# Optimization experiments

Measured on AMD Instinct MI355X. Metric: run time of the kernel, lower is better.

## Reference

```python
import jax, jax.numpy as jnp
import numpy as np

N_NODES = 46080   # 512 graphs x 90 nodes
NPG = 90          # nodes per graph (AAL atlas)
G = 512           # number of graphs
E = 737280        # edges (degree 16)
IN_DIM = 90
H = 64            # hidden_channels
K = 70            # sort-pool k


def setup_inputs() -> dict:
    key = jax.random.key(0)
    ks = jax.random.split(key, 12)
    x = jax.random.normal(ks[0], (N_NODES, IN_DIM), dtype=jnp.float32)
    # intra-graph random edges: src/dst within each graph's 90-node block
    gidx = jnp.repeat(jnp.arange(G, dtype=jnp.int64), E // G) * NPG
    src = jax.random.randint(ks[1], (E,), 0, NPG, dtype=jnp.int64) + gidx
    dst = jax.random.randint(ks[2], (E,), 0, NPG, dtype=jnp.int64) + gidx
    edge_index = jnp.stack([src, dst])
    edge_weight = jax.random.uniform(ks[3], (E,), dtype=jnp.float32)
    batch = jnp.repeat(jnp.arange(G, dtype=jnp.int64), NPG)
    s1 = 1.0 / np.sqrt(IN_DIM)
    s2 = 1.0 / np.sqrt(H)
    sk = 1.0 / np.sqrt(H * K)
    W1 = jax.random.uniform(ks[4], (IN_DIM, H), jnp.float32, -s1, s1)
    b1 = jnp.zeros((H,), jnp.float32)
    W2 = jax.random.uniform(ks[5], (H, H), jnp.float32, -s2, s2)
    b2 = jnp.zeros((H,), jnp.float32)
    lw1 = jax.random.uniform(ks[6], (H * K, H), jnp.float32, -sk, sk)
    lb1 = jax.random.uniform(ks[7], (H,), jnp.float32, -sk, sk)
    lw2 = jax.random.uniform(ks[8], (H, 1), jnp.float32, -s2, s2)
    lb2 = jax.random.uniform(ks[9], (1,), jnp.float32, -s2, s2)
    return {"x": x, "edge_index": edge_index, "edge_weight": edge_weight,
            "batch": batch, "W1": W1, "b1": b1, "W2": W2, "b2": b2,
            "lw1": lw1, "lb1": lb1, "lw2": lw2, "lb2": lb2}


def _gcn_conv(x, W, b, src, dst, ew, n):
    # PyG GCNConv: add self-loops (weight 1), symmetric normalization,
    # message = norm * (x @ W)[src], scatter-add to dst, add bias.
    xw = x @ W
    loop = jnp.arange(n)
    src_f = jnp.concatenate([src, loop])
    dst_f = jnp.concatenate([dst, loop])
    ew_f = jnp.concatenate([ew, jnp.ones((n,), x.dtype)])
    deg = jax.ops.segment_sum(ew_f, dst_f, num_segments=n)
    dinv = jnp.where(deg > 0, jax.lax.rsqrt(jnp.maximum(deg, 1e-12)), 0.0)
    norm = dinv[src_f] * ew_f * dinv[dst_f]
    msg = xw[src_f] * norm[:, None]          # [E+n, H] irregular gather
    out = jax.ops.segment_sum(msg, dst_f, num_segments=n)
    return out + b


def reference(x, edge_index, edge_weight, batch, W1, b1, W2, b2, lw1, lb1, lw2, lb2):
    src, dst = edge_index[0], edge_index[1]
    h1 = _gcn_conv(x, W1, b1, src, dst, edge_weight, N_NODES)
    x_train = h1
    h = jax.nn.relu(h1)
    h2 = _gcn_conv(h, W2, b2, src, dst, edge_weight, N_NODES)
    # global_sort_pool: per graph, sort nodes descending by last channel, keep top K.
    # batch is contiguous with NPG nodes/graph, so a reshape is exact.
    hg = h2.reshape(G, NPG, H)
    order = jnp.argsort(-hg[:, :, -1], axis=1)          # [G, NPG] descending
    hs = jnp.take_along_axis(hg, order[:, :, None], axis=1)
    pooled = hs[:, :K, :].reshape(G, K * H)
    # F.dropout(p=0.5, training=False) -> identity at inference
    z = pooled @ lw1 + lb1
    z = z @ lw2 + lb2
    out = jax.nn.sigmoid(z).squeeze(-1)                  # [G]
    return out, x_train
```

## Files before the change

kernel.cpp:

```cpp
#include <hip/hip_runtime.h>


#define NG      512
#define NPG     90
#define EPG     1440
#define IN_DIM  90
#define HD      64
#define KP      70
#define E_TOT   (NG*EPG)
#define NT      512

__global__ __launch_bounds__(NT, 4) void dgcnn_fused(
    const float* __restrict__ x,
    const int*   __restrict__ ei,
    const float* __restrict__ ew,
    const float* __restrict__ W1,
    const float* __restrict__ b1,
    const float* __restrict__ W2,
    const float* __restrict__ b2,
    const float* __restrict__ lw1,
    const float* __restrict__ lb1,
    const float* __restrict__ lw2,
    const float* __restrict__ lb2,
    float* __restrict__ out,
    float* __restrict__ xtrain)
{
    __shared__ float sB[NPG*HD];
    __shared__ float sC[NPG*HD];
    __shared__ float sW2[HD*HD];
    __shared__ float s_deg[NPG];
    __shared__ float s_dinv[NPG];
    __shared__ int   s_indeg[NPG];
    __shared__ int   s_rowstart[NPG+1];
    __shared__ int   s_cursor[NPG];
    __shared__ float2 s_cpack[EPG];
    __shared__ int   s_ranknode[KP];
    __shared__ float s_zpart[NT];

    const int g = blockIdx.x;
    const int t = threadIdx.x;
    const int j = t & 63;
    const int grp = t >> 6;
    const int ebase = g*EPG;
    const int nbase = g*NPG;

    if (t < NPG) { s_deg[t] = 1.0f; s_indeg[t] = 0; }
    __syncthreads();

    for (int e = t; e < EPG; e += NT) {
        int d = ei[E_TOT + ebase + e] - nbase;
        float w = ew[ebase + e];
        atomicAdd(&s_deg[d], w);
        atomicAdd(&s_indeg[d], 1);
    }
    __syncthreads();

    if (t < NPG) s_dinv[t] = rsqrtf(fmaxf(s_deg[t], 1e-12f));
    if (t <= NPG) {
        int acc = 0;
        for (int i = 0; i < t; ++i) acc += s_indeg[i];
        s_rowstart[t] = acc;
        if (t < NPG) s_cursor[t] = acc;
    }
    __syncthreads();

    for (int e = t; e < EPG; e += NT) {
        int s = ei[ebase + e] - nbase;
        int d = ei[E_TOT + ebase + e] - nbase;
        float w = ew[ebase + e];
        int pos = atomicAdd(&s_cursor[d], 1);
        s_cpack[pos] = make_float2(s_dinv[s] * w * s_dinv[d], __int_as_float(s));
    }
    for (int i4 = t; i4 < IN_DIM*HD/4; i4 += NT)
        ((float4*)sC)[i4] = ((const float4*)W1)[i4];
    __syncthreads();

    const float* xg = x + (size_t)nbase * IN_DIM;
    for (int it = 0; it < 3; ++it) {
        int r0 = it*32 + grp*4;
        int rr0 = min(r0+0, NPG-1), rr1 = min(r0+1, NPG-1);
        int rr2 = min(r0+2, NPG-1), rr3 = min(r0+3, NPG-1);
        const float2* xp0 = (const float2*)(xg + rr0*IN_DIM);
        const float2* xp1 = (const float2*)(xg + rr1*IN_DIM);
        const float2* xp2 = (const float2*)(xg + rr2*IN_DIM);
        const float2* xp3 = (const float2*)(xg + rr3*IN_DIM);
        float a0 = 0.f, a1 = 0.f, a2 = 0.f, a3 = 0.f;
        #pragma unroll 9
        for (int kh = 0; kh < IN_DIM/2; ++kh) {
            float w0 = sC[(2*kh)*HD + j];
            float w1 = sC[(2*kh+1)*HD + j];
            float2 v0 = xp0[kh], v1 = xp1[kh], v2 = xp2[kh], v3 = xp3[kh];
            a0 += v0.x*w0 + v0.y*w1;
            a1 += v1.x*w0 + v1.y*w1;
            a2 += v2.x*w0 + v2.y*w1;
            a3 += v3.x*w0 + v3.y*w1;
        }
        if (r0+0 < NPG) sB[(r0+0)*HD + j] = a0;
        if (r0+1 < NPG) sB[(r0+1)*HD + j] = a1;
        if (r0+2 < NPG) sB[(r0+2)*HD + j] = a2;
        if (r0+3 < NPG) sB[(r0+3)*HD + j] = a3;
    }
    __syncthreads();

    for (int o = t; o < NPG*HD; o += NT) {
        int d = o >> 6, c = o & 63;
        float dv = s_dinv[d];
        float a = dv*dv*sB[o];
        int p0 = s_rowstart[d], p1 = s_rowstart[d+1];
        for (int p = p0; p < p1; ++p) {
            float2 pk = s_cpack[p];
            a += pk.x * sB[__float_as_int(pk.y)*HD + c];
        }
        sC[o] = a + b1[c];
    }
    __syncthreads();

    float* xt = xtrain + (size_t)nbase * HD;
    for (int i4 = t; i4 < NPG*HD/4; i4 += NT) {
        float4 v = ((float4*)sC)[i4];
        ((float4*)xt)[i4] = v;
        v.x = fmaxf(v.x, 0.f); v.y = fmaxf(v.y, 0.f);
        v.z = fmaxf(v.z, 0.f); v.w = fmaxf(v.w, 0.f);
        ((float4*)sC)[i4] = v;
    }
    for (int i4 = t; i4 < HD*HD/4; i4 += NT)
        ((float4*)sW2)[i4] = ((const float4*)W2)[i4];
    __syncthreads();

    for (int it = 0; it < 3; ++it) {
        int r0 = it*32 + grp*4;
        int rr0 = min(r0+0, NPG-1), rr1 = min(r0+1, NPG-1);
        int rr2 = min(r0+2, NPG-1), rr3 = min(r0+3, NPG-1);
        float a0 = 0.f, a1 = 0.f, a2 = 0.f, a3 = 0.f;
        #pragma unroll 4
        for (int k4 = 0; k4 < HD/4; ++k4) {
            int k = k4*4;
            float4 h0 = *(const float4*)&sC[rr0*HD + k];
            float4 h1 = *(const float4*)&sC[rr1*HD + k];
            float4 h2 = *(const float4*)&sC[rr2*HD + k];
            float4 h3 = *(const float4*)&sC[rr3*HD + k];
            float w0 = sW2[(k+0)*HD + j];
            float w1 = sW2[(k+1)*HD + j];
            float w2 = sW2[(k+2)*HD + j];
            float w3 = sW2[(k+3)*HD + j];
            a0 += h0.x*w0 + h0.y*w1 + h0.z*w2 + h0.w*w3;
            a1 += h1.x*w0 + h1.y*w1 + h1.z*w2 + h1.w*w3;
            a2 += h2.x*w0 + h2.y*w1 + h2.z*w2 + h2.w*w3;
            a3 += h3.x*w0 + h3.y*w1 + h3.z*w2 + h3.w*w3;
        }
        if (r0+0 < NPG) sB[(r0+0)*HD + j] = a0;
        if (r0+1 < NPG) sB[(r0+1)*HD + j] = a1;
        if (r0+2 < NPG) sB[(r0+2)*HD + j] = a2;
        if (r0+3 < NPG) sB[(r0+3)*HD + j] = a3;
    }
    __syncthreads();

    for (int o = t; o < NPG*HD; o += NT) {
        int d = o >> 6, c = o & 63;
        float dv = s_dinv[d];
        float a = dv*dv*sB[o];
        int p0 = s_rowstart[d], p1 = s_rowstart[d+1];
        for (int p = p0; p < p1; ++p) {
            float2 pk = s_cpack[p];
            a += pk.x * sB[__float_as_int(pk.y)*HD + c];
        }
        sC[o] = a + b2[c];
    }
    __syncthreads();

    if (t < NPG) {
        float vi = sC[t*HD + (HD-1)];
        int rank = 0;
        for (int jj = 0; jj < NPG; ++jj) {
            float vj = sC[jj*HD + (HD-1)];
            rank += (vj > vi) || (vj == vi && jj < t);
        }
        if (rank < KP) s_ranknode[rank] = t;
    }
    __syncthreads();

    {
        float partial = 0.f;
        for (int k = grp; k < KP; k += 8) {
            int node = s_ranknode[k];
            const float4* prow = (const float4*)&sC[node*HD];
            const float* wrow = lw1 + (size_t)(k*HD)*HD + j;
            #pragma unroll 4
            for (int c4 = 0; c4 < HD/4; ++c4) {
                float4 pv = prow[c4];
                int c = c4*4;
                partial += pv.x * wrow[(size_t)(c+0)*HD];
                partial += pv.y * wrow[(size_t)(c+1)*HD];
                partial += pv.z * wrow[(size_t)(c+2)*HD];
                partial += pv.w * wrow[(size_t)(c+3)*HD];
            }
        }
        s_zpart[t] = partial;
    }
    __syncthreads();

    if (t < HD) {
        float z1 = lb1[t];
        #pragma unroll
        for (int m = 0; m < NT/HD; ++m) z1 += s_zpart[t + m*HD];
        float zz = z1 * lw2[t];
        #pragma unroll
        for (int off = 32; off > 0; off >>= 1) zz += __shfl_down(zz, off, 64);
        if (t == 0) out[g] = 1.0f / (1.0f + expf(-(zz + lb2[0])));
    }
}

extern "C" void kernel_launch(void* const* d_in, const int* in_sizes, int n_in,
                              void* d_out, int out_size, void* d_ws, size_t ws_size,
                              hipStream_t stream) {
    const float* x   = (const float*)d_in[0];
    const int*   ei  = (const int*)  d_in[1];
    const float* ew  = (const float*)d_in[2];
    const float* W1  = (const float*)d_in[4];
    const float* b1  = (const float*)d_in[5];
    const float* W2  = (const float*)d_in[6];
    const float* b2  = (const float*)d_in[7];
    const float* lw1 = (const float*)d_in[8];
    const float* lb1 = (const float*)d_in[9];
    const float* lw2 = (const float*)d_in[10];
    const float* lb2 = (const float*)d_in[11];

    float* out    = (float*)d_out;
    float* xtrain = out + NG;

    dgcnn_fused<<<NG, NT, 0, stream>>>(x, ei, ew, W1, b1, W2, b2,
                                       lw1, lb1, lw2, lb2, out, xtrain);
}
```

Baseline: 192.7 us.

## Fold the two dense head layers into one vector and slim the shared-memory footprint

A small pre-kernel folds lw1·lw2 and the biases into one effective weight vector, since no nonlinearity sits between the two head layers. The per-graph head then becomes a single dot product instead of a 4480x64 matrix-vector product streamed from global memory. Shared memory is also reduced to allow more blocks per CU: edge norm and source index are packed into one 32-bit word by truncating the low 7 mantissa bits of the norm, the W2 shared copy is dropped in favour of global/L1 reads, and the xtrain store is fused into the aggregation loop. Edge data is kept in registers between passes. The costs are an extra launch, a small loss of precision in the norm, and a changed summation order.

```diff
diff --git a/kernel.cpp b/kernel.cpp
--- a/kernel.cpp
+++ b/kernel.cpp
@@ -10,7 +10,30 @@
 #define E_TOT   (NG*EPG)
 #define NT      512
 
-__global__ __launch_bounds__(NT, 4) void dgcnn_fused(
+__global__ __launch_bounds__(256) void weff_fold(
+    const float* __restrict__ lw1, const float* __restrict__ lb1,
+    const float* __restrict__ lw2, const float* __restrict__ lb2,
+    float* __restrict__ ws)
+{
+    int i = blockIdx.x*256 + threadIdx.x;
+    if (i < KP*HD) {
+        const float4* row = (const float4*)(lw1 + (size_t)i*HD);
+        const float4* w   = (const float4*)lw2;
+        float s = 0.f;
+        #pragma unroll
+        for (int j4 = 0; j4 < HD/4; ++j4) {
+            float4 r = row[j4], v = w[j4];
+            s += r.x*v.x + r.y*v.y + r.z*v.z + r.w*v.w;
+        }
+        ws[i] = s;
+    } else if (i == KP*HD) {
+        float s = lb2[0];
+        for (int j = 0; j < HD; ++j) s += lb1[j]*lw2[j];
+        ws[KP*HD] = s;
+    }
+}
+
+__global__ __launch_bounds__(NT, 6) void dgcnn_fused(
     const float* __restrict__ x,
     const int*   __restrict__ ei,
     const float* __restrict__ ew,
@@ -18,24 +41,18 @@
     const float* __restrict__ b1,
     const float* __restrict__ W2,
     const float* __restrict__ b2,
-    const float* __restrict__ lw1,
-    const float* __restrict__ lb1,
-    const float* __restrict__ lw2,
-    const float* __restrict__ lb2,
+    const float* __restrict__ weff,
     float* __restrict__ out,
     float* __restrict__ xtrain)
 {
     __shared__ float sB[NPG*HD];
     __shared__ float sC[NPG*HD];
-    __shared__ float sW2[HD*HD];
-    __shared__ float s_deg[NPG];
     __shared__ float s_dinv[NPG];
-    __shared__ int   s_indeg[NPG];
+    __shared__ int   s_cursor[NPG];
     __shared__ int   s_rowstart[NPG+1];
-    __shared__ int   s_cursor[NPG];
-    __shared__ float2 s_cpack[EPG];
+    __shared__ unsigned s_epack[EPG];
     __shared__ int   s_ranknode[KP];
-    __shared__ float s_zpart[NT];
+    __shared__ float s_red[8];
 
     const int g = blockIdx.x;
     const int t = threadIdx.x;
@@ -44,35 +61,46 @@
     const int ebase = g*EPG;
     const int nbase = g*NPG;
 
-    if (t < NPG) { s_deg[t] = 1.0f; s_indeg[t] = 0; }
-    __syncthreads();
-
-    for (int e = t; e < EPG; e += NT) {
-        int d = ei[E_TOT + ebase + e] - nbase;
-        float w = ew[ebase + e];
-        atomicAdd(&s_deg[d], w);
-        atomicAdd(&s_indeg[d], 1);
-    }
-    __syncthreads();
-
-    if (t < NPG) s_dinv[t] = rsqrtf(fmaxf(s_deg[t], 1e-12f));
+    if (t < NPG) { s_dinv[t] = 1.0f; s_cursor[t] = 0; }
+    __syncthreads();
+
+    int   e_s[3], e_d[3];
+    float e_w[3];
+    #pragma unroll
+    for (int m = 0; m < 3; ++m) {
+        int e = t + m*NT;
+        if (e < EPG) {
+            e_s[m] = ei[ebase + e] - nbase;
+            e_d[m] = ei[E_TOT + ebase + e] - nbase;
+            e_w[m] = ew[ebase + e];
+            atomicAdd(&s_dinv[e_d[m]], e_w[m]);
+            atomicAdd(&s_cursor[e_d[m]], 1);
+        }
+    }
+    for (int i4 = t; i4 < IN_DIM*HD/4; i4 += NT)
+        ((float4*)sC)[i4] = ((const float4*)W1)[i4];
+    __syncthreads();
+
+    if (t < NPG) s_dinv[t] = rsqrtf(fmaxf(s_dinv[t], 1e-12f));
     if (t <= NPG) {
         int acc = 0;
-        for (int i = 0; i < t; ++i) acc += s_indeg[i];
+        for (int i = 0; i < t; ++i) acc += s_cursor[i];
         s_rowstart[t] = acc;
-        if (t < NPG) s_cursor[t] = acc;
-    }
-    __syncthreads();
-
-    for (int e = t; e < EPG; e += NT) {
-        int s = ei[ebase + e] - nbase;
-        int d = ei[E_TOT + ebase + e] - nbase;
-        float w = ew[ebase + e];
-        int pos = atomicAdd(&s_cursor[d], 1);
-        s_cpack[pos] = make_float2(s_dinv[s] * w * s_dinv[d], __int_as_float(s));
-    }
-    for (int i4 = t; i4 < IN_DIM*HD/4; i4 += NT)
-        ((float4*)sC)[i4] = ((const float4*)W1)[i4];
+    }
+    __syncthreads();
+    if (t < NPG) s_cursor[t] = s_rowstart[t];
+    __syncthreads();
+
+    #pragma unroll
+    for (int m = 0; m < 3; ++m) {
+        int e = t + m*NT;
+        if (e < EPG) {
+            int s = e_s[m], d = e_d[m];
+            float nrm = s_dinv[s] * e_w[m] * s_dinv[d];
+            int pos = atomicAdd(&s_cursor[d], 1);
+            s_epack[pos] = (__float_as_uint(nrm) & ~127u) | (unsigned)s;
+        }
+    }
     __syncthreads();
 
     const float* xg = x + (size_t)nbase * IN_DIM;
@@ -102,29 +130,20 @@
     }
     __syncthreads();
 
+    float* xt = xtrain + (size_t)nbase * HD;
     for (int o = t; o < NPG*HD; o += NT) {
         int d = o >> 6, c = o & 63;
         float dv = s_dinv[d];
         float a = dv*dv*sB[o];
         int p0 = s_rowstart[d], p1 = s_rowstart[d+1];
         for (int p = p0; p < p1; ++p) {
-            float2 pk = s_cpack[p];
-            a += pk.x * sB[__float_as_int(pk.y)*HD + c];
-        }
-        sC[o] = a + b1[c];
-    }
-    __syncthreads();
-
-    float* xt = xtrain + (size_t)nbase * HD;
-    for (int i4 = t; i4 < NPG*HD/4; i4 += NT) {
-        float4 v = ((float4*)sC)[i4];
-        ((float4*)xt)[i4] = v;
-        v.x = fmaxf(v.x, 0.f); v.y = fmaxf(v.y, 0.f);
-        v.z = fmaxf(v.z, 0.f); v.w = fmaxf(v.w, 0.f);
-        ((float4*)sC)[i4] = v;
-    }
-    for (int i4 = t; i4 < HD*HD/4; i4 += NT)
-        ((float4*)sW2)[i4] = ((const float4*)W2)[i4];
+            unsigned u = s_epack[p];
+            a += __uint_as_float(u & ~127u) * sB[(int)(u & 127u)*HD + c];
+        }
+        a += b1[c];
+        xt[o] = a;
+        sC[o] = fmaxf(a, 0.f);
+    }
     __syncthreads();
 
     for (int it = 0; it < 3; ++it) {
@@ -139,10 +158,10 @@
             float4 h1 = *(const float4*)&sC[rr1*HD + k];
             float4 h2 = *(const float4*)&sC[rr2*HD + k];
             float4 h3 = *(const float4*)&sC[rr3*HD + k];
-            float w0 = sW2[(k+0)*HD + j];
-            float w1 = sW2[(k+1)*HD + j];
-            float w2 = sW2[(k+2)*HD + j];
-            float w3 = sW2[(k+3)*HD + j];
+            float w0 = W2[(k+0)*HD + j];
+            float w1 = W2[(k+1)*HD + j];
+            float w2 = W2[(k+2)*HD + j];
+            float w3 = W2[(k+3)*HD + j];
             a0 += h0.x*w0 + h0.y*w1 + h0.z*w2 + h0.w*w3;
             a1 += h1.x*w0 + h1.y*w1 + h1.z*w2 + h1.w*w3;
             a2 += h2.x*w0 + h2.y*w1 + h2.z*w2 + h2.w*w3;
@@ -161,8 +180,8 @@
         float a = dv*dv*sB[o];
         int p0 = s_rowstart[d], p1 = s_rowstart[d+1];
         for (int p = p0; p < p1; ++p) {
-            float2 pk = s_cpack[p];
-            a += pk.x * sB[__float_as_int(pk.y)*HD + c];
+            unsigned u = s_epack[p];
+            a += __uint_as_float(u & ~127u) * sB[(int)(u & 127u)*HD + c];
         }
         sC[o] = a + b2[c];
     }
@@ -179,34 +198,24 @@
     }
     __syncthreads();
 
-    {
-        float partial = 0.f;
-        for (int k = grp; k < KP; k += 8) {
-            int node = s_ranknode[k];
-            const float4* prow = (const float4*)&sC[node*HD];
-            const float* wrow = lw1 + (size_t)(k*HD)*HD + j;
-            #pragma unroll 4
-            for (int c4 = 0; c4 < HD/4; ++c4) {
-                float4 pv = prow[c4];
-                int c = c4*4;
-                partial += pv.x * wrow[(size_t)(c+0)*HD];
-                partial += pv.y * wrow[(size_t)(c+1)*HD];
-                partial += pv.z * wrow[(size_t)(c+2)*HD];
-                partial += pv.w * wrow[(size_t)(c+3)*HD];
-            }
-        }
-        s_zpart[t] = partial;
-    }
-    __syncthreads();
-
-    if (t < HD) {
-        float z1 = lb1[t];
+    float part = 0.f;
+    #pragma unroll
+    for (int m = 0; m < 9; ++m) {
+        int i = t + m*NT;
+        if (i < KP*HD) {
+            int k = i >> 6, c = i & 63;
+            part += weff[i] * sC[s_ranknode[k]*HD + c];
+        }
+    }
+    #pragma unroll
+    for (int off = 32; off > 0; off >>= 1) part += __shfl_down(part, off, 64);
+    if (j == 0) s_red[grp] = part;
+    __syncthreads();
+    if (t == 0) {
+        float zz = weff[KP*HD];
         #pragma unroll
-        for (int m = 0; m < NT/HD; ++m) z1 += s_zpart[t + m*HD];
-        float zz = z1 * lw2[t];
-        #pragma unroll
-        for (int off = 32; off > 0; off >>= 1) zz += __shfl_down(zz, off, 64);
-        if (t == 0) out[g] = 1.0f / (1.0f + expf(-(zz + lb2[0])));
+        for (int m = 0; m < 8; ++m) zz += s_red[m];
+        out[g] = 1.0f / (1.0f + expf(-zz));
     }
 }
 
@@ -225,9 +234,11 @@
     const float* lw2 = (const float*)d_in[10];
     const float* lb2 = (const float*)d_in[11];
 
+    float* ws     = (float*)d_ws;
     float* out    = (float*)d_out;
     float* xtrain = out + NG;
 
+    weff_fold<<<(KP*HD + 256)/256, 256, 0, stream>>>(lw1, lb1, lw2, lb2, ws);
     dgcnn_fused<<<NG, NT, 0, stream>>>(x, ei, ew, W1, b1, W2, b2,
-                                       lw1, lb1, lw2, lb2, out, xtrain);
+                                       ws, out, xtrain);
 }
```

After: 209.8 us. 1.09x slower.
